# Kernel tuning notes

Measured on AMD Instinct MI355X. Metric: run time of the kernel, lower is better.

Reference implementation:

```python
import jax, jax.numpy as jnp
import numpy as np

TAU = 2.0
V_TH = 1.0
V_RESET = 0.0
SG_ALPHA = 4.0  # spikingjelly default Sigmoid surrogate alpha

@jax.custom_vjp
def heaviside_sg(x):
    return (x >= 0).astype(x.dtype)

def _hs_fwd(x):
    return heaviside_sg(x), x

def _hs_bwd(x, g):
    s = jax.nn.sigmoid(SG_ALPHA * x)
    return (g * SG_ALPHA * s * (1.0 - s),)

heaviside_sg.defvjp(_hs_fwd, _hs_bwd)

def lif_multistep(x):
    # x: [T, B, N, D]; hard-reset LIF, detach_reset=True
    def step(v, xt):
        v = v + (xt - (v - V_RESET)) / TAU  # membrane charge
        spike = heaviside_sg(v - V_TH)
        sd = jax.lax.stop_gradient(spike)   # detach_reset
        v = (1.0 - sd) * v + sd * V_RESET   # hard reset
        return v, spike
    v0 = jnp.zeros_like(x[0])
    _, spikes = jax.lax.scan(step, v0, x)
    return spikes  # [T, B, N, D]

def setup_inputs() -> dict:
    key = jax.random.key(0)
    k1, k2 = jax.random.split(key)
    T, B, N, D, C = 4, 64, 196, 512, 1000
    x = jax.random.normal(k1, (T, B, N, D), dtype=jnp.float32)
    W = jax.random.normal(k2, (C, D), dtype=jnp.float32) * (1.0 / np.sqrt(D))
    b = jnp.zeros((C,), dtype=jnp.float32)
    return {"x": x, "W": W, "b": b}

def reference(x, W, b):
    s = lif_multistep(x)                         # [T,B,N,D] spikes in {0,1}
    y = jnp.einsum('tbnd,cd->tbnc', s, W) + b    # linear head
    return y
```

## Files before the change

### kernel.cpp

```cpp
#include <hip/hip_runtime.h>
#include <hip/hip_bf16.h>
#include <stdint.h>


typedef __attribute__((ext_vector_type(8))) short bf16x8;
typedef __attribute__((ext_vector_type(4))) float f32x4;

#define AS1(p) ((const __attribute__((address_space(1))) void*)(p))
#define AS3(p) ((__attribute__((address_space(3))) void*)(p))

static constexpr int     T_STEPS = 4;
static constexpr int64_t ESP     = 6422528;
static constexpr int     K_DIM   = 512;
static constexpr int     C_DIM   = 1000;
static constexpr int64_t M_ROWS  = 50176;

static constexpr int LIF_BLOCKS = 3136;
static constexpr int WCV_BLOCKS = 512;

__device__ __forceinline__ unsigned short f2bf(float f) {
  unsigned int u = __float_as_uint(f);
  u += 0x7FFFu + ((u >> 16) & 1u);
  return (unsigned short)(u >> 16);
}

__global__ void lifw_kernel(const float* __restrict__ x,
                            unsigned short* __restrict__ S,
                            const float* __restrict__ W,
                            unsigned short* __restrict__ Wb) {
  const int b = blockIdx.x;
  if (b >= LIF_BLOCKS) {
    const int idx = (b - LIF_BLOCKS) * 256 + threadIdx.x;
    const int64_t base = (int64_t)idx * 4;
    const int row = (int)(base >> 9);
    ushort4 o;
    if (row < C_DIM) {
      const float4 wv = *(const float4*)(W + base);
      o.x = f2bf(wv.x); o.y = f2bf(wv.y); o.z = f2bf(wv.z); o.w = f2bf(wv.w);
    } else {
      o.x = o.y = o.z = o.w = 0;
    }
    *(ushort4*)(Wb + base) = o;
    return;
  }
  const int64_t tb = (int64_t)b * 256 + threadIdx.x;
#pragma unroll
  for (int it = 0; it < 2; ++it) {
    const int64_t s0 = (tb + (int64_t)it * LIF_BLOCKS * 256) << 2;
    float v[4] = {0.f, 0.f, 0.f, 0.f};
#pragma unroll
    for (int t = 0; t < T_STEPS; ++t) {
      const float4 xt = *(const float4*)(x + (int64_t)t * ESP + s0);
      const float xa[4] = {xt.x, xt.y, xt.z, xt.w};
      ushort4 sp;
      unsigned short* spp = &sp.x;
#pragma unroll
      for (int j = 0; j < 4; ++j) {
        v[j] = v[j] + (xa[j] - v[j]) * 0.5f;
        const bool fire = (v[j] >= 1.0f);
        spp[j] = fire ? (unsigned short)0x3F80 : (unsigned short)0;
        if (fire) v[j] = 0.0f;
      }
      *(ushort4*)(S + (int64_t)t * ESP + s0) = sp;
    }
  }
}

__global__ __launch_bounds__(256, 4) void gemm_kernel(
    const unsigned short* __restrict__ S,
    const unsigned short* __restrict__ Wb,
    const float* __restrict__ bias,
    float* __restrict__ Y) {
  __shared__ __attribute__((aligned(16))) unsigned short As[128 * 64];
  __shared__ __attribute__((aligned(16))) unsigned short Bs[128 * 64];

  const int tid  = threadIdx.x;
  const int lane = tid & 63;
  const int wid  = tid >> 6;
  const int wm   = wid >> 1;
  const int wn   = wid & 1;

  const int bid   = blockIdx.x;
  const int xcd   = bid & 7;
  const int j     = bid >> 3;
  const int mtile = xcd * 49 + (j >> 3);
  const int ntile = j & 7;
  const int64_t row0 = (int64_t)mtile * 128;
  const int     c0   = ntile * 128;

  const int srow = lane >> 3;
  const int skb  = ((lane & 7) ^ srow) << 4;

  const char* Sg = (const char*)S;
  const char* Wg = (const char*)Wb;
  char* Ab = (char*)As;
  char* Bb = (char*)Bs;

  f32x4 acc[4][4] = {};

  const int lr = lane & 15;
  const int lk = (lane >> 4) * 16;

  for (int t = 0; t < 8; ++t) {
    const int k0 = t * 64;
#pragma unroll
    for (int i = 0; i < 4; ++i) {
      const int rr = i * 32 + wid * 8;
      __builtin_amdgcn_global_load_lds(
          AS1(Sg + ((row0 + rr + srow) * (int64_t)K_DIM + k0) * 2 + skb),
          AS3(Ab + rr * 128), 16, 0, 0);
    }
#pragma unroll
    for (int i = 0; i < 4; ++i) {
      const int rr = i * 32 + wid * 8;
      __builtin_amdgcn_global_load_lds(
          AS1(Wg + (((int64_t)c0 + rr + srow) * K_DIM + k0) * 2 + skb),
          AS3(Bb + rr * 128), 16, 0, 0);
    }
    __syncthreads();

#pragma unroll
    for (int half = 0; half < 2; ++half) {
      const int kb = half * 64 + lk;
      bf16x8 afr[4], bfr[4];
#pragma unroll
      for (int mi = 0; mi < 4; ++mi) {
        const int r = wm * 64 + mi * 16 + lr;
        afr[mi] = *(const bf16x8*)(Ab + r * 128 + (kb ^ ((r & 7) << 4)));
      }
#pragma unroll
      for (int nj = 0; nj < 4; ++nj) {
        const int r = wn * 64 + nj * 16 + lr;
        bfr[nj] = *(const bf16x8*)(Bb + r * 128 + (kb ^ ((r & 7) << 4)));
      }
#pragma unroll
      for (int mi = 0; mi < 4; ++mi)
#pragma unroll
        for (int nj = 0; nj < 4; ++nj)
          acc[mi][nj] = __builtin_amdgcn_mfma_f32_16x16x32_bf16(
              afr[mi], bfr[nj], acc[mi][nj], 0, 0, 0);
    }
    __syncthreads();
  }

  float bvn[4];
#pragma unroll
  for (int nj = 0; nj < 4; ++nj) {
    const int c = c0 + wn * 64 + nj * 16 + lr;
    bvn[nj] = (c < C_DIM) ? bias[c] : 0.f;
  }

  char* obuf = (char*)&As[0];
  const int cwb = (C_DIM - c0 < 128 ? C_DIM - c0 : 128) * 4;
  const int rwp = wid * 2;
  const int rsel = lane >> 5;
  const int cb  = (lane & 31) * 16;

#pragma unroll
  for (int slice = 0; slice < 2; ++slice) {
    __syncthreads();
    if (wm == slice) {
#pragma unroll
      for (int mi = 0; mi < 4; ++mi) {
#pragma unroll
        for (int nj = 0; nj < 4; ++nj) {
          const int cl = (wn * 64 + nj * 16 + lr) * 4;
#pragma unroll
          for (int r = 0; r < 4; ++r) {
            const int rl = mi * 16 + (lane >> 4) * 4 + r;
            *(float*)(obuf + ((rl * 512 + cl) ^ ((rl & 7) << 4))) =
                acc[mi][nj][r] + bvn[nj];
          }
        }
      }
    }
    __syncthreads();
#pragma unroll
    for (int pass = 0; pass < 8; ++pass) {
      const int rl = pass * 8 + rwp + rsel;
      const f32x4 v =
          *(const f32x4*)(obuf + ((rl * 512 + cb) ^ ((rl & 7) << 4)));
      if (cb < cwb) {
        const int64_t m = row0 + slice * 64 + rl;
        f32x4* dst = (f32x4*)((char*)(Y + m * (int64_t)C_DIM) + c0 * 4 + cb);
        __builtin_nontemporal_store(v, dst);
      }
    }
  }
}

extern "C" void kernel_launch(void* const* d_in, const int* in_sizes, int n_in,
                              void* d_out, int out_size, void* d_ws, size_t ws_size,
                              hipStream_t stream) {
  const float* x = (const float*)d_in[0];
  const float* W = (const float*)d_in[1];
  const float* b = (const float*)d_in[2];
  float* Y = (float*)d_out;

  unsigned short* S  = (unsigned short*)d_ws;
  unsigned short* Wb = S + (size_t)M_ROWS * K_DIM;

  hipLaunchKernelGGL(lifw_kernel, dim3(LIF_BLOCKS + WCV_BLOCKS), dim3(256), 0,
                     stream, x, S, W, Wb);
  hipLaunchKernelGGL(gemm_kernel, dim3(3136), dim3(256), 0, stream, S, Wb, b, Y);
}
```

Baseline: 94.36 us.

## Use 256x256 tiles with 8 waves and double-buffered LDS prefetch pipeline

The GEMM moves from 128x128 tiles with 4 waves and a single LDS buffer to 256x256 tiles with 8 waves. Global-to-LDS loads are now double-buffered and issued in quarter-stages interleaved with MFMA phases, using explicit vmcnt waits and barriers plus setprio around the MFMA bursts. The aim is to hide load latency and raise operand reuse per byte loaded. The cost is one block per CU, 128KB of LDS, and a 256-wide N tile that wastes more padded columns since 1000 is not a multiple of 256.

```diff
diff --git a/kernel.cpp b/kernel.cpp
--- a/kernel.cpp
+++ b/kernel.cpp
@@ -66,122 +66,157 @@
   }
 }
 
-__global__ __launch_bounds__(256, 4) void gemm_kernel(
+__global__ __launch_bounds__(512, 1) void gemm_kernel(
     const unsigned short* __restrict__ S,
     const unsigned short* __restrict__ Wb,
     const float* __restrict__ bias,
     float* __restrict__ Y) {
-  __shared__ __attribute__((aligned(16))) unsigned short As[128 * 64];
-  __shared__ __attribute__((aligned(16))) unsigned short Bs[128 * 64];
+  __shared__ __attribute__((aligned(16))) unsigned short As[2][256 * 64];
+  __shared__ __attribute__((aligned(16))) unsigned short Bs[2][256 * 64];
 
   const int tid  = threadIdx.x;
   const int lane = tid & 63;
   const int wid  = tid >> 6;
-  const int wm   = wid >> 1;
-  const int wn   = wid & 1;
+  const int wm   = wid >> 2;
+  const int wn   = wid & 3;
 
   const int bid   = blockIdx.x;
-  const int xcd   = bid & 7;
-  const int j     = bid >> 3;
-  const int mtile = xcd * 49 + (j >> 3);
-  const int ntile = j & 7;
-  const int64_t row0 = (int64_t)mtile * 128;
-  const int     c0   = ntile * 128;
+  const int swz   = (bid & 7) * 98 + (bid >> 3);
+  const int mtile = swz >> 2;
+  const int ntile = swz & 3;
+  const int64_t row0 = (int64_t)mtile * 256;
+  const int     c0   = ntile * 256;
 
   const int srow = lane >> 3;
   const int skb  = ((lane & 7) ^ srow) << 4;
 
   const char* Sg = (const char*)S;
   const char* Wg = (const char*)Wb;
-  char* Ab = (char*)As;
-  char* Bb = (char*)Bs;
-
-  f32x4 acc[4][4] = {};
+
+  auto stage = [&](int tile, int j) {
+    const int buf = tile & 1;
+    const int k0  = tile * 64;
+    const int hh  = (j >> 1) * 128;
+    if ((j & 1) == 0) {
+#pragma unroll
+      for (int i = 0; i < 2; ++i) {
+        const int rr = hh + i * 64 + wid * 8;
+        __builtin_amdgcn_global_load_lds(
+            AS1(Sg + ((row0 + rr + srow) * (int64_t)K_DIM + k0) * 2 + skb),
+            AS3((char*)&As[buf][0] + rr * 128), 16, 0, 0);
+      }
+    } else {
+#pragma unroll
+      for (int i = 0; i < 2; ++i) {
+        const int rr = hh + i * 64 + wid * 8;
+        __builtin_amdgcn_global_load_lds(
+            AS1(Wg + (((int64_t)c0 + rr + srow) * K_DIM + k0) * 2 + skb),
+            AS3((char*)&Bs[buf][0] + rr * 128), 16, 0, 0);
+      }
+    }
+  };
+
+  f32x4 acc[2][2][4][2] = {};
 
   const int lr = lane & 15;
   const int lk = (lane >> 4) * 16;
 
+  stage(0, 0); stage(0, 1); stage(0, 3); stage(0, 2);
+  stage(1, 0); stage(1, 1);
+  asm volatile("s_waitcnt vmcnt(4)" ::: "memory");
+  __builtin_amdgcn_s_barrier();
+
+#pragma unroll
   for (int t = 0; t < 8; ++t) {
-    const int k0 = t * 64;
-#pragma unroll
-    for (int i = 0; i < 4; ++i) {
-      const int rr = i * 32 + wid * 8;
-      __builtin_amdgcn_global_load_lds(
-          AS1(Sg + ((row0 + rr + srow) * (int64_t)K_DIM + k0) * 2 + skb),
-          AS3(Ab + rr * 128), 16, 0, 0);
-    }
-#pragma unroll
-    for (int i = 0; i < 4; ++i) {
-      const int rr = i * 32 + wid * 8;
-      __builtin_amdgcn_global_load_lds(
-          AS1(Wg + (((int64_t)c0 + rr + srow) * K_DIM + k0) * 2 + skb),
-          AS3(Bb + rr * 128), 16, 0, 0);
-    }
+    const int cur = t & 1;
+    const char* Ab = (const char*)&As[cur][0];
+    const char* Bb = (const char*)&Bs[cur][0];
+#pragma unroll
+    for (int p = 0; p < 4; ++p) {
+      const int hp = p >> 1, vp = p & 1;
+      bf16x8 afr[4][2], bfr[2][2];
+#pragma unroll
+      for (int mi2 = 0; mi2 < 4; ++mi2) {
+        const int r = hp * 128 + wm * 64 + mi2 * 16 + lr;
+#pragma unroll
+        for (int ks = 0; ks < 2; ++ks)
+          afr[mi2][ks] = *(const bf16x8*)(
+              Ab + r * 128 + ((ks * 64 + lk) ^ ((r & 7) << 4)));
+      }
+#pragma unroll
+      for (int nj2 = 0; nj2 < 2; ++nj2) {
+        const int r = vp * 128 + wn * 32 + nj2 * 16 + lr;
+#pragma unroll
+        for (int ks = 0; ks < 2; ++ks)
+          bfr[nj2][ks] = *(const bf16x8*)(
+              Bb + r * 128 + ((ks * 64 + lk) ^ ((r & 7) << 4)));
+      }
+      if (p == 0)      { if (t + 1 < 8) stage(t + 1, 3); }
+      else if (p == 1) { if (t + 1 < 8) stage(t + 1, 2); }
+      else if (p == 2) { if (t + 2 < 8) stage(t + 2, 0); }
+      else             { if (t + 2 < 8) stage(t + 2, 1); }
+      __builtin_amdgcn_s_barrier();
+      asm volatile("s_waitcnt lgkmcnt(0)" ::: "memory");
+      __builtin_amdgcn_sched_barrier(0);
+      __builtin_amdgcn_s_setprio(1);
+#pragma unroll
+      for (int mi2 = 0; mi2 < 4; ++mi2)
+#pragma unroll
+        for (int nj2 = 0; nj2 < 2; ++nj2)
+#pragma unroll
+          for (int ks = 0; ks < 2; ++ks)
+            acc[hp][vp][mi2][nj2] = __builtin_amdgcn_mfma_f32_16x16x32_bf16(
+                afr[mi2][ks], bfr[nj2][ks], acc[hp][vp][mi2][nj2], 0, 0, 0);
+      __builtin_amdgcn_s_setprio(0);
+      if (p == 3) {
+        if (t <= 5)      asm volatile("s_waitcnt vmcnt(4)" ::: "memory");
+        else if (t == 6) asm volatile("s_waitcnt vmcnt(0)" ::: "memory");
+      }
+      __builtin_amdgcn_s_barrier();
+    }
+  }
+
+  float bvn[2][2];
+#pragma unroll
+  for (int vp = 0; vp < 2; ++vp)
+#pragma unroll
+    for (int nj2 = 0; nj2 < 2; ++nj2) {
+      const int c = c0 + vp * 128 + wn * 32 + nj2 * 16 + lr;
+      bvn[vp][nj2] = (c < C_DIM) ? bias[c] : 0.f;
+    }
+
+  char* obuf = (char*)&As[0][0];
+  const int cw4 = (C_DIM - c0 < 256 ? C_DIM - c0 : 256) * 4;
+  const int cb  = lane * 16;
+
+#pragma unroll
+  for (int s = 0; s < 4; ++s) {
     __syncthreads();
-
-#pragma unroll
-    for (int half = 0; half < 2; ++half) {
-      const int kb = half * 64 + lk;
-      bf16x8 afr[4], bfr[4];
-#pragma unroll
-      for (int mi = 0; mi < 4; ++mi) {
-        const int r = wm * 64 + mi * 16 + lr;
-        afr[mi] = *(const bf16x8*)(Ab + r * 128 + (kb ^ ((r & 7) << 4)));
-      }
-#pragma unroll
-      for (int nj = 0; nj < 4; ++nj) {
-        const int r = wn * 64 + nj * 16 + lr;
-        bfr[nj] = *(const bf16x8*)(Bb + r * 128 + (kb ^ ((r & 7) << 4)));
-      }
-#pragma unroll
-      for (int mi = 0; mi < 4; ++mi)
-#pragma unroll
-        for (int nj = 0; nj < 4; ++nj)
-          acc[mi][nj] = __builtin_amdgcn_mfma_f32_16x16x32_bf16(
-              afr[mi], bfr[nj], acc[mi][nj], 0, 0, 0);
+    if (wm == (s & 1)) {
+      const int hp = s >> 1;
+#pragma unroll
+      for (int mi2 = 0; mi2 < 4; ++mi2)
+#pragma unroll
+        for (int vp = 0; vp < 2; ++vp)
+#pragma unroll
+          for (int nj2 = 0; nj2 < 2; ++nj2) {
+            const int cl = (vp * 128 + wn * 32 + nj2 * 16 + lr) * 4;
+#pragma unroll
+            for (int r = 0; r < 4; ++r) {
+              const int rl = mi2 * 16 + (lane >> 4) * 4 + r;
+              *(float*)(obuf + ((rl * 1024 + cl) ^ ((rl & 7) << 4))) =
+                  acc[hp][vp][mi2][nj2][r] + bvn[vp][nj2];
+            }
+          }
     }
     __syncthreads();
-  }
-
-  float bvn[4];
-#pragma unroll
-  for (int nj = 0; nj < 4; ++nj) {
-    const int c = c0 + wn * 64 + nj * 16 + lr;
-    bvn[nj] = (c < C_DIM) ? bias[c] : 0.f;
-  }
-
-  char* obuf = (char*)&As[0];
-  const int cwb = (C_DIM - c0 < 128 ? C_DIM - c0 : 128) * 4;
-  const int rwp = wid * 2;
-  const int rsel = lane >> 5;
-  const int cb  = (lane & 31) * 16;
-
-#pragma unroll
-  for (int slice = 0; slice < 2; ++slice) {
-    __syncthreads();
-    if (wm == slice) {
-#pragma unroll
-      for (int mi = 0; mi < 4; ++mi) {
-#pragma unroll
-        for (int nj = 0; nj < 4; ++nj) {
-          const int cl = (wn * 64 + nj * 16 + lr) * 4;
-#pragma unroll
-          for (int r = 0; r < 4; ++r) {
-            const int rl = mi * 16 + (lane >> 4) * 4 + r;
-            *(float*)(obuf + ((rl * 512 + cl) ^ ((rl & 7) << 4))) =
-                acc[mi][nj][r] + bvn[nj];
-          }
-        }
-      }
-    }
-    __syncthreads();
 #pragma unroll
     for (int pass = 0; pass < 8; ++pass) {
-      const int rl = pass * 8 + rwp + rsel;
+      const int rl = pass * 8 + wid;
       const f32x4 v =
-          *(const f32x4*)(obuf + ((rl * 512 + cb) ^ ((rl & 7) << 4)));
-      if (cb < cwb) {
-        const int64_t m = row0 + slice * 64 + rl;
+          *(const f32x4*)(obuf + ((rl * 1024 + cb) ^ ((rl & 7) << 4)));
+      if (cb < cw4) {
+        const int64_t m = row0 + (s >> 1) * 128 + (s & 1) * 64 + rl;
         f32x4* dst = (f32x4*)((char*)(Y + m * (int64_t)C_DIM) + c0 * 4 + cb);
         __builtin_nontemporal_store(v, dst);
       }
@@ -202,5 +237,5 @@
 
   hipLaunchKernelGGL(lifw_kernel, dim3(LIF_BLOCKS + WCV_BLOCKS), dim3(256), 0,
                      stream, x, S, W, Wb);
-  hipLaunchKernelGGL(gemm_kernel, dim3(3136), dim3(256), 0, stream, S, Wb, b, Y);
-}
+  hipLaunchKernelGGL(gemm_kernel, dim3(784), dim3(512), 0, stream, S, Wb, b, Y);
+}
```

Result: slower. 131.2 us (+39.0%).
